# Performance work log

Measured on AMD Instinct MI355X. Metric: run time of the kernel, lower is better.

Reference implementation:

```python
import jax, jax.numpy as jnp
import numpy as np

B, S, D, H = 4, 2048, 1024, 16
HD = D // H  # head_dim = 64


def setup_inputs() -> dict:
    key = jax.random.key(0)
    ks = jax.random.split(key, 10)
    sc = 0.02
    return {
        "data": jax.random.normal(ks[0], (B, S, D), jnp.float32),
        "context": jax.random.normal(ks[1], (B, S, D), jnp.float32),
        "Wq": jax.random.normal(ks[2], (D, D), jnp.float32) * sc,
        "bq": jnp.zeros((D,), jnp.float32),
        "Wk": jax.random.normal(ks[3], (D, D), jnp.float32) * sc,
        "bk": jnp.zeros((D,), jnp.float32),
        "Wv": jax.random.normal(ks[4], (D, D), jnp.float32) * sc,
        "bv": jnp.zeros((D,), jnp.float32),
        "Wo": jax.random.normal(ks[5], (D, D), jnp.float32) * sc,
        "bo": jnp.zeros((D,), jnp.float32),
    }


def reference(data, context, Wq, bq, Wk, bk, Wv, bv, Wo, bo):
    # Q/K/V projections (nn.Linear: x @ W^T + b; here weights stored as [in, out])
    Q = data @ Wq + bq            # [B,S,D]
    K = context @ Wk + bk
    V = context @ Wv + bv
    # split heads -> [B,H,S,HD]
    Q = Q.reshape(B, S, H, HD).transpose(0, 2, 1, 3)
    K = K.reshape(B, S, H, HD).transpose(0, 2, 1, 3)
    V = V.reshape(B, S, H, HD).transpose(0, 2, 1, 3)
    scale = jnp.sqrt(jnp.asarray(HD, Q.dtype))
    Z = jnp.einsum("bhqd,bhkd->bhqk", Q, K) / scale   # [B,H,S,S]
    # causal mask: row >= col allowed
    row = jnp.arange(S)[:, None]
    col = jnp.arange(S)[None, :]
    Z = jnp.where(row >= col, Z, jnp.asarray(-jnp.inf, Z.dtype))
    Z = jax.nn.softmax(Z, axis=-1)
    out = jnp.einsum("bhqk,bhkd->bhqd", Z, V)         # [B,H,S,HD]
    out = out.transpose(0, 2, 1, 3).reshape(B, S, D)
    return out @ Wo + bo
```

## Files before the change

### kernel.cpp

```cpp
#include <hip/hip_runtime.h>
#include <hip/hip_bf16.h>

#define B_ 4
#define S_ 2048
#define D_ 1024
#define H_ 16
#define HD_ 64
#define M_ (B_*S_)
#define NTOK (M_*D_)

typedef __bf16 bf16;
typedef __bf16 bf16v4 __attribute__((ext_vector_type(4)));
typedef __bf16 bf16v8 __attribute__((ext_vector_type(8)));
typedef float f32x4 __attribute__((ext_vector_type(4)));
typedef float f32x16 __attribute__((ext_vector_type(16)));

#define GLDS(gp, lp) __builtin_amdgcn_global_load_lds( \
    (const __attribute__((address_space(1))) void*)(gp), \
    (__attribute__((address_space(3))) void*)(lp), 16, 0, 0)

__global__ void prep_kernel(const float* __restrict__ data, const float* __restrict__ ctx,
                            bf16* __restrict__ dataB, bf16* __restrict__ ctxB,
                            const float* __restrict__ W0, const float* __restrict__ W1,
                            const float* __restrict__ W2, const float* __restrict__ W3,
                            bf16* __restrict__ T0, bf16* __restrict__ T1,
                            bf16* __restrict__ T2, bf16* __restrict__ T3,
                            float s0) {
    int bid = blockIdx.x;
    if (bid < 8192) {
        int i = (bid * 256 + (int)threadIdx.x) * 8;
        const float* src; bf16* dst;
        if (i < NTOK) { src = data + i; dst = dataB + i; }
        else          { src = ctx + (i - NTOK); dst = ctxB + (i - NTOK); }
        const float4* p = reinterpret_cast<const float4*>(src);
        float4 x = p[0], y = p[1];
        bf16v8 o;
        o[0] = (bf16)x.x; o[1] = (bf16)x.y; o[2] = (bf16)x.z; o[3] = (bf16)x.w;
        o[4] = (bf16)y.x; o[5] = (bf16)y.y; o[6] = (bf16)y.z; o[7] = (bf16)y.w;
        *reinterpret_cast<bf16v8*>(dst) = o;
    } else {
        __shared__ float tile[32][33];
        int local = bid - 8192;
        int which = local >> 10;
        int rem = local & 1023;
        const float* W = which == 0 ? W0 : which == 1 ? W1 : which == 2 ? W2 : W3;
        bf16* Wt       = which == 0 ? T0 : which == 1 ? T1 : which == 2 ? T2 : T3;
        float scale    = which == 0 ? s0 : 1.f;
        int nb = (rem & 31) * 32, kb = (rem >> 5) * 32;
        int t = threadIdx.x;
        int c = t & 31, r0 = t >> 5;
        for (int i = 0; i < 4; ++i) {
            int r = r0 + i * 8;
            tile[r][c] = W[(size_t)(kb + r) * D_ + nb + c];
        }
        __syncthreads();
        for (int i = 0; i < 4; ++i) {
            int r = r0 + i * 8;
            Wt[(size_t)(nb + r) * D_ + kb + c] = (bf16)(tile[c][r] * scale);
        }
    }
}

__global__ __launch_bounds__(256) void gemm_qkvo_kernel(
        const bf16* __restrict__ dataB, const bf16* __restrict__ ctxB, const bf16* __restrict__ Ob,
        const bf16* __restrict__ WqT, const bf16* __restrict__ WkT,
        const bf16* __restrict__ WvT, const bf16* __restrict__ WoT,
        const float* __restrict__ bq, const float* __restrict__ bk,
        const float* __restrict__ bv, const float* __restrict__ bo,
        bf16* __restrict__ Qb, bf16* __restrict__ Kb, bf16* __restrict__ Vt,
        float* __restrict__ outp, float qscale, int zofs) {
    __shared__ bf16 Asm[128 * 64];
    __shared__ bf16 Bsm[128 * 64];
    int z = blockIdx.z + zofs;
    const bf16* A; const bf16* Bt; const float* bias; float bscale = 1.f;
    if (z == 0)      { A = dataB; Bt = WqT; bias = bq; bscale = qscale; }
    else if (z == 1) { A = ctxB;  Bt = WkT; bias = bk; }
    else if (z == 2) { A = ctxB;  Bt = WvT; bias = bv; }
    else             { A = Ob;    Bt = WoT; bias = bo; }

    int mb = blockIdx.x * 128, nb = blockIdx.y * 128;
    int t = threadIdx.x, l = t & 63, w = t >> 6;
    int wr = w >> 1, wc = w & 1;
    int lg = l >> 4, lr = l & 15;
    f32x4 acc[4][4] = {};
    int srow = t >> 3;
    int schk = t & 7;
    for (int k0 = 0; k0 < D_; k0 += 64) {
        __syncthreads();
        #pragma unroll
        for (int p = 0; p < 4; ++p) {
            int row = p * 32 + srow;
            int ca = schk ^ (row & 7);
            GLDS(&A[(size_t)(mb + row) * D_ + k0 + ca * 8], &Asm[(size_t)(p * 256 + t) * 8]);
            GLDS(&Bt[(size_t)(nb + row) * D_ + k0 + ca * 8], &Bsm[(size_t)(p * 256 + t) * 8]);
        }
        __syncthreads();
        #pragma unroll
        for (int kk = 0; kk < 2; ++kk) {
            bf16v8 af[4], bfv[4];
            #pragma unroll
            for (int i = 0; i < 4; ++i) {
                int ra = wr * 64 + i * 16 + lr;
                af[i]  = *(const bf16v8*)&Asm[ra * 64 + (((kk * 4 + lg) ^ (ra & 7)) * 8)];
                int rb = wc * 64 + i * 16 + lr;
                bfv[i] = *(const bf16v8*)&Bsm[rb * 64 + (((kk * 4 + lg) ^ (rb & 7)) * 8)];
            }
            #pragma unroll
            for (int i = 0; i < 4; ++i)
                #pragma unroll
                for (int j = 0; j < 4; ++j)
                    acc[i][j] = __builtin_amdgcn_mfma_f32_16x16x32_bf16(af[i], bfv[j], acc[i][j], 0, 0, 0);
        }
    }
    #pragma unroll
    for (int i = 0; i < 4; ++i)
        #pragma unroll
        for (int j = 0; j < 4; ++j) {
            int col = nb + wc * 64 + j * 16 + lr;
            float bvv = bias[col] * bscale;
            int row0 = mb + wr * 64 + i * 16 + lg * 4;
            if (z == 2) {
                int b = row0 >> 11, s = row0 & 2047;
                int bh = b * 16 + (col >> 6), hd = col & 63;
                bf16v4 ov;
                #pragma unroll
                for (int r = 0; r < 4; ++r) ov[r] = (bf16)(acc[i][j][r] + bvv);
                *(bf16v4*)&Vt[((size_t)bh * 64 + hd) * 2048 + s] = ov;
            } else if (z == 3) {
                #pragma unroll
                for (int r = 0; r < 4; ++r)
                    outp[(size_t)(row0 + r) * D_ + col] = acc[i][j][r] + bvv;
            } else {
                bf16* dst = (z == 0) ? Qb : Kb;
                #pragma unroll
                for (int r = 0; r < 4; ++r)
                    dst[(size_t)(row0 + r) * D_ + col] = (bf16)(acc[i][j][r] + bvv);
            }
        }
}

__global__ __launch_bounds__(256, 2) void attn_kernel(const bf16* __restrict__ Q,
                                                      const bf16* __restrict__ Kb,
                                                      const bf16* __restrict__ Vt,
                                                      bf16* __restrict__ O) {
    __shared__ bf16 Ksm[2][64 * 64];
    __shared__ bf16 Vsm[2][64 * 64];

    int id = (int)blockIdx.x;
    int bh = id & 63;
    int qi = (S_ / 128 - 1) - (id >> 6);
    int qb = qi * 128;
    int b = bh >> 4, h = bh & 15;
    int t = threadIdx.x, w = t >> 6, l = t & 63;
    int ln = l & 31, hi = l >> 5;
    int qwave = qb + w * 32;
    int q = qwave + ln;

    const bf16* kbase = Kb + (size_t)(b * S_) * D_ + h * HD_;
    const bf16* vbase = Vt + (size_t)bh * HD_ * S_;
    const bf16* qptr  = Q + (size_t)(b * S_ + q) * D_ + h * HD_;

    bf16v8 qf[4];
    #pragma unroll
    for (int c = 0; c < 4; ++c)
        qf[c] = *(const bf16v8*)(qptr + c * 16 + hi * 8);

    bf16v8 ones;
    #pragma unroll
    for (int e = 0; e < 8; ++e) ones[e] = (bf16)1.0f;

    f32x16 o0 = {}, o1 = {};
    f32x16 ls = {};

    int srow = t >> 3, schk = t & 7;
    int nT = 2 * qi + 2;

    auto stage = [&](int kv0, int bufsel) {
        #pragma unroll
        for (int p = 0; p < 2; ++p) {
            int row = p * 32 + srow;
            int cs = schk ^ (row & 7);
            GLDS(kbase + (size_t)(kv0 + row) * D_ + cs * 8, &Ksm[bufsel][p * 2048 + t * 8]);
            GLDS(vbase + (size_t)row * S_ + kv0 + cs * 8,   &Vsm[bufsel][p * 2048 + t * 8]);
        }
    };

    stage(0, 0);
    for (int tt = 0; tt < nT; ++tt) {
        int cur = tt & 1;
        int kv0 = tt * 64;
        __syncthreads();
        if (tt + 1 < nT) stage(kv0 + 64, cur ^ 1);
        if (kv0 > qwave + 31) continue;

        f32x16 st0 = {}, st1 = {};
        __builtin_amdgcn_s_setprio(1);
        #pragma unroll
        for (int c = 0; c < 4; ++c) {
            int r0 = ln;
            bf16v8 kf0 = *(const bf16v8*)&Ksm[cur][r0 * 64 + (((2 * c + hi) ^ (r0 & 7)) * 8)];
            st0 = __builtin_amdgcn_mfma_f32_32x32x16_bf16(kf0, qf[c], st0, 0, 0, 0);
            int r1 = 32 + ln;
            bf16v8 kf1 = *(const bf16v8*)&Ksm[cur][r1 * 64 + (((2 * c + hi) ^ (r1 & 7)) * 8)];
            st1 = __builtin_amdgcn_mfma_f32_32x32x16_bf16(kf1, qf[c], st1, 0, 0, 0);
        }
        __builtin_amdgcn_s_setprio(0);

        if (kv0 + 63 > qwave) {
            #pragma unroll
            for (int rg = 0; rg < 16; ++rg) {
                int kvo = (rg & 3) + 8 * (rg >> 2) + 4 * hi;
                if (kv0 + kvo > q)      st0[rg] = -__builtin_inff();
                if (kv0 + 32 + kvo > q) st1[rg] = -__builtin_inff();
            }
        }

        #pragma unroll
        for (int i = 0; i < 16; ++i) {
            st0[i] = __builtin_exp2f(st0[i]);
            st1[i] = __builtin_exp2f(st1[i]);
        }

        uint32_t x0[4][2], x1[4][2];
        #pragma unroll
        for (int j = 0; j < 4; ++j) {
            asm("v_cvt_pk_bf16_f32 %0, %1, %2" : "=v"(x0[j][0]) : "v"(st0[4*j+0]), "v"(st0[4*j+1]));
            asm("v_cvt_pk_bf16_f32 %0, %1, %2" : "=v"(x0[j][1]) : "v"(st0[4*j+2]), "v"(st0[4*j+3]));
            asm("v_cvt_pk_bf16_f32 %0, %1, %2" : "=v"(x1[j][0]) : "v"(st1[4*j+0]), "v"(st1[4*j+1]));
            asm("v_cvt_pk_bf16_f32 %0, %1, %2" : "=v"(x1[j][1]) : "v"(st1[4*j+2]), "v"(st1[4*j+3]));
        }
        union PB { uint32_t u[4]; bf16v8 v; };
        PB pb[4];
        #pragma unroll
        for (int c = 0; c < 4; ++c) {
            uint32_t (*xs)[2] = (c >> 1) ? x1 : x0;
            int cp = c & 1;
            #pragma unroll
            for (int d = 0; d < 2; ++d) {
                uint32_t own_lo = xs[2 * cp][d];
                uint32_t own_hi = xs[2 * cp + 1][d];
                uint32_t par_lo = __shfl_xor(own_lo, 32, 64);
                uint32_t par_hi = __shfl_xor(own_hi, 32, 64);
                pb[c].u[d]     = hi ? par_hi : own_lo;
                pb[c].u[2 + d] = hi ? own_hi : par_lo;
            }
        }

        __builtin_amdgcn_s_setprio(1);
        #pragma unroll
        for (int c = 0; c < 4; ++c) {
            int r0 = ln;
            bf16v8 va0 = *(const bf16v8*)&Vsm[cur][r0 * 64 + (((2 * c + hi) ^ (r0 & 7)) * 8)];
            o0 = __builtin_amdgcn_mfma_f32_32x32x16_bf16(va0, pb[c].v, o0, 0, 0, 0);
            int r1 = 32 + ln;
            bf16v8 va1 = *(const bf16v8*)&Vsm[cur][r1 * 64 + (((2 * c + hi) ^ (r1 & 7)) * 8)];
            o1 = __builtin_amdgcn_mfma_f32_32x32x16_bf16(va1, pb[c].v, o1, 0, 0, 0);
            ls = __builtin_amdgcn_mfma_f32_32x32x16_bf16(ones, pb[c].v, ls, 0, 0, 0);
        }
        __builtin_amdgcn_s_setprio(0);
    }

    float li = 1.f / ls[0];
    bf16* obase = O + (size_t)(b * S_ + q) * D_ + h * HD_;
    #pragma unroll
    for (int j = 0; j < 4; ++j) {
        bf16v4 ov;
        #pragma unroll
        for (int r = 0; r < 4; ++r) ov[r] = (bf16)(o0[4 * j + r] * li);
        *(bf16v4*)(obase + 8 * j + 4 * hi) = ov;
    }
    #pragma unroll
    for (int j = 0; j < 4; ++j) {
        bf16v4 ov;
        #pragma unroll
        for (int r = 0; r < 4; ++r) ov[r] = (bf16)(o1[4 * j + r] * li);
        *(bf16v4*)(obase + 32 + 8 * j + 4 * hi) = ov;
    }
}

extern "C" void kernel_launch(void* const* d_in, const int* in_sizes, int n_in,
                              void* d_out, int out_size, void* d_ws, size_t ws_size,
                              hipStream_t stream) {
    const float* data    = (const float*)d_in[0];
    const float* context = (const float*)d_in[1];
    const float* Wq = (const float*)d_in[2];
    const float* bq = (const float*)d_in[3];
    const float* Wk = (const float*)d_in[4];
    const float* bk = (const float*)d_in[5];
    const float* Wv = (const float*)d_in[6];
    const float* bv = (const float*)d_in[7];
    const float* Wo = (const float*)d_in[8];
    const float* bo = (const float*)d_in[9];
    float* out = (float*)d_out;

    char* ws = (char*)d_ws;
    size_t off = 0;
    auto alloc = [&](size_t bytes) { void* p = ws + off; off += (bytes + 255) & ~255ull; return p; };
    bf16* dataB = (bf16*)alloc((size_t)M_ * D_ * 2);
    bf16* ctxB  = (bf16*)alloc((size_t)M_ * D_ * 2);
    bf16* WqT   = (bf16*)alloc((size_t)D_ * D_ * 2);
    bf16* WkT   = (bf16*)alloc((size_t)D_ * D_ * 2);
    bf16* WvT   = (bf16*)alloc((size_t)D_ * D_ * 2);
    bf16* WoT   = (bf16*)alloc((size_t)D_ * D_ * 2);
    bf16* Qb    = (bf16*)alloc((size_t)M_ * D_ * 2);
    bf16* Kb    = (bf16*)alloc((size_t)M_ * D_ * 2);
    bf16* Vt    = (bf16*)alloc((size_t)M_ * D_ * 2);
    bf16* Ob    = ctxB;

    const float qscale = 0.125f * 1.44269504088896340736f;

    prep_kernel<<<12288, 256, 0, stream>>>(data, context, dataB, ctxB,
                                           Wq, Wk, Wv, Wo, WqT, WkT, WvT, WoT, qscale);

    gemm_qkvo_kernel<<<dim3(M_ / 128, D_ / 128, 3), 256, 0, stream>>>(
        dataB, ctxB, Ob, WqT, WkT, WvT, WoT, bq, bk, bv, bo, Qb, Kb, Vt, out, qscale, 0);

    attn_kernel<<<dim3(S_ / 128 * B_ * H_), 256, 0, stream>>>(Qb, Kb, Vt, Ob);

    gemm_qkvo_kernel<<<dim3(M_ / 128, D_ / 128, 1), 256, 0, stream>>>(
        dataB, ctxB, Ob, WqT, WkT, WvT, WoT, bq, bk, bv, bo, Qb, Kb, Vt, out, qscale, 3);
}
```

Measured before the change: 175.2 us.

## Add 256x256 double-buffered pipelined QKV GEMM with 8 waves

Replaces the QKV projection GEMM with a new kernel using 256x256 tiles, 512 threads and a double-buffered LDS pipeline. Async global-to-LDS loads are interleaved with MFMA phases, with explicit vmcnt waits, barriers and raised scheduling priority around the MFMA blocks. The intent is to hide memory latency and raise arithmetic intensity per block. The output projection moves to its own simpler kernel. The larger tiles use 128 KB of LDS per block and shrink the grid, which risks lower occupancy and tail imbalance, and the hand-written waitcnt counts must match the issued loads exactly.

Measured after the change: 186.0 us. +6.1%, slower.

```diff
diff --git a/kernel.cpp b/kernel.cpp
--- a/kernel.cpp
+++ b/kernel.cpp
@@ -61,23 +61,144 @@
     }
 }
 
-__global__ __launch_bounds__(256) void gemm_qkvo_kernel(
-        const bf16* __restrict__ dataB, const bf16* __restrict__ ctxB, const bf16* __restrict__ Ob,
-        const bf16* __restrict__ WqT, const bf16* __restrict__ WkT,
-        const bf16* __restrict__ WvT, const bf16* __restrict__ WoT,
-        const float* __restrict__ bq, const float* __restrict__ bk,
-        const float* __restrict__ bv, const float* __restrict__ bo,
-        bf16* __restrict__ Qb, bf16* __restrict__ Kb, bf16* __restrict__ Vt,
-        float* __restrict__ outp, float qscale, int zofs) {
+__global__ __launch_bounds__(512, 2) void gemm_qkv8_kernel(
+        const bf16* __restrict__ dataB, const bf16* __restrict__ ctxB,
+        const bf16* __restrict__ WqT, const bf16* __restrict__ WkT, const bf16* __restrict__ WvT,
+        const float* __restrict__ bq, const float* __restrict__ bk, const float* __restrict__ bv,
+        bf16* __restrict__ Qb, bf16* __restrict__ Kb, bf16* __restrict__ Vt, float qscale) {
+    __shared__ bf16 Asm[2][256 * 64];
+    __shared__ bf16 Bsm[2][256 * 64];
+    int z = blockIdx.z;
+    const bf16* A  = (z == 0) ? dataB : ctxB;
+    const bf16* Bt = (z == 0) ? WqT : (z == 1) ? WkT : WvT;
+    const float* bias = (z == 0) ? bq : (z == 1) ? bk : bv;
+    float bscale = (z == 0) ? qscale : 1.f;
+
+    int mb = blockIdx.x * 256, nb = blockIdx.y * 256;
+    int t = threadIdx.x, l = t & 63, w = t >> 6;
+    int wr = w >> 2, wc = w & 3;
+    int lg = l >> 4, lr = l & 15;
+    int srow = t >> 3, schk = t & 7;
+
+    f32x4 acc[2][2][4][2] = {};
+
+    auto stageA = [&](int tile, int g) {
+        int buf = tile & 1;
+        #pragma unroll
+        for (int p64 = 0; p64 < 2; ++p64) {
+            int row = p64 * 128 + g * 64 + srow;
+            int cs = schk ^ (row & 7);
+            GLDS(A + (size_t)(mb + row) * D_ + tile * 64 + cs * 8,
+                 &Asm[buf][row * 64 + schk * 8]);
+        }
+    };
+    auto stageB = [&](int tile, int g) {
+        int buf = tile & 1;
+        #pragma unroll
+        for (int p64 = 0; p64 < 2; ++p64) {
+            int v = p64 * 64 + srow;
+            int row = (v >> 5) * 64 + g * 32 + (v & 31);
+            int cs = schk ^ (row & 7);
+            GLDS(Bt + (size_t)(nb + row) * D_ + tile * 64 + cs * 8,
+                 &Bsm[buf][row * 64 + schk * 8]);
+        }
+    };
+
+    stageA(0, 0); stageB(0, 0); stageA(0, 1); stageB(0, 1); stageA(1, 0); stageB(1, 0);
+    asm volatile("s_waitcnt vmcnt(8)" ::: "memory");
+    __builtin_amdgcn_s_barrier();
+
+    for (int it = 0; it < 8; ++it) {
+        int b1 = 2 * it + 1, a2 = 2 * it + 2, b2 = 2 * it + 3;
+        #pragma unroll
+        for (int p = 0; p < 8; ++p) {
+            const int tsel = p >> 2;
+            const int qa = (p >> 1) & 1, qb = p & 1;
+
+            bf16v8 af[4][2], bfv[2][2];
+            #pragma unroll
+            for (int i4 = 0; i4 < 4; ++i4) {
+                int ra = wr * 128 + qa * 64 + i4 * 16 + lr;
+                #pragma unroll
+                for (int kk = 0; kk < 2; ++kk)
+                    af[i4][kk] = *(const bf16v8*)&Asm[tsel][ra * 64 + (((kk * 4 + lg) ^ (ra & 7)) * 8)];
+            }
+            #pragma unroll
+            for (int j2 = 0; j2 < 2; ++j2) {
+                int rb = wc * 64 + qb * 32 + j2 * 16 + lr;
+                #pragma unroll
+                for (int kk = 0; kk < 2; ++kk)
+                    bfv[j2][kk] = *(const bf16v8*)&Bsm[tsel][rb * 64 + (((kk * 4 + lg) ^ (rb & 7)) * 8)];
+            }
+
+            if (p == 0)      stageA(b1, 1);
+            else if (p == 1) stageB(b1, 1);
+            else if (p == 2) { if (a2 < 16) stageA(a2, 0); }
+            else if (p == 3) { if (a2 < 16) stageB(a2, 0); }
+            else if (p == 4) { if (a2 < 16) stageA(a2, 1); }
+            else if (p == 5) { if (a2 < 16) stageB(a2, 1); }
+            else if (p == 6) { if (b2 < 16) stageA(b2, 0); }
+            else             { if (b2 < 16) stageB(b2, 0); }
+
+            if (p == 0) asm volatile("s_waitcnt vmcnt(6)" ::: "memory");
+            if (p == 3) {
+                if (it == 7) asm volatile("s_waitcnt vmcnt(0)" ::: "memory");
+                else         asm volatile("s_waitcnt vmcnt(8)" ::: "memory");
+            }
+            if (p == 4 && it < 7) asm volatile("s_waitcnt vmcnt(6)" ::: "memory");
+            if (p == 7 && it < 7) asm volatile("s_waitcnt vmcnt(8)" ::: "memory");
+
+            __builtin_amdgcn_s_barrier();
+            asm volatile("s_waitcnt lgkmcnt(0)" ::: "memory");
+            __builtin_amdgcn_sched_barrier(0);
+            __builtin_amdgcn_s_setprio(1);
+            #pragma unroll
+            for (int kk = 0; kk < 2; ++kk)
+                #pragma unroll
+                for (int i4 = 0; i4 < 4; ++i4)
+                    #pragma unroll
+                    for (int j2 = 0; j2 < 2; ++j2)
+                        acc[qa][qb][i4][j2] = __builtin_amdgcn_mfma_f32_16x16x32_bf16(
+                            af[i4][kk], bfv[j2][kk], acc[qa][qb][i4][j2], 0, 0, 0);
+            __builtin_amdgcn_s_setprio(0);
+            __builtin_amdgcn_s_barrier();
+        }
+    }
+
+    #pragma unroll
+    for (int qa = 0; qa < 2; ++qa)
+        #pragma unroll
+        for (int qb = 0; qb < 2; ++qb)
+            #pragma unroll
+            for (int i4 = 0; i4 < 4; ++i4)
+                #pragma unroll
+                for (int j2 = 0; j2 < 2; ++j2) {
+                    int col = nb + wc * 64 + qb * 32 + j2 * 16 + lr;
+                    float bvv = bias[col] * bscale;
+                    int row0 = mb + wr * 128 + qa * 64 + i4 * 16 + lg * 4;
+                    f32x4 a = acc[qa][qb][i4][j2];
+                    if (z == 2) {
+                        int bb = row0 >> 11, s = row0 & 2047;
+                        int bh = bb * 16 + (col >> 6), hd = col & 63;
+                        bf16v4 ov;
+                        #pragma unroll
+                        for (int r = 0; r < 4; ++r) ov[r] = (bf16)(a[r] + bvv);
+                        *(bf16v4*)&Vt[((size_t)bh * 64 + hd) * 2048 + s] = ov;
+                    } else {
+                        bf16* dst = (z == 0) ? Qb : Kb;
+                        #pragma unroll
+                        for (int r = 0; r < 4; ++r)
+                            dst[(size_t)(row0 + r) * D_ + col] = (bf16)(a[r] + bvv);
+                    }
+                }
+}
+
+__global__ __launch_bounds__(256) void gemm_o_kernel(const bf16* __restrict__ Ob,
+                                                     const bf16* __restrict__ WoT,
+                                                     const float* __restrict__ bo,
+                                                     float* __restrict__ outp) {
     __shared__ bf16 Asm[128 * 64];
     __shared__ bf16 Bsm[128 * 64];
-    int z = blockIdx.z + zofs;
-    const bf16* A; const bf16* Bt; const float* bias; float bscale = 1.f;
-    if (z == 0)      { A = dataB; Bt = WqT; bias = bq; bscale = qscale; }
-    else if (z == 1) { A = ctxB;  Bt = WkT; bias = bk; }
-    else if (z == 2) { A = ctxB;  Bt = WvT; bias = bv; }
-    else             { A = Ob;    Bt = WoT; bias = bo; }
-
     int mb = blockIdx.x * 128, nb = blockIdx.y * 128;
     int t = threadIdx.x, l = t & 63, w = t >> 6;
     int wr = w >> 1, wc = w & 1;
@@ -91,8 +212,8 @@
         for (int p = 0; p < 4; ++p) {
             int row = p * 32 + srow;
             int ca = schk ^ (row & 7);
-            GLDS(&A[(size_t)(mb + row) * D_ + k0 + ca * 8], &Asm[(size_t)(p * 256 + t) * 8]);
-            GLDS(&Bt[(size_t)(nb + row) * D_ + k0 + ca * 8], &Bsm[(size_t)(p * 256 + t) * 8]);
+            GLDS(&Ob[(size_t)(mb + row) * D_ + k0 + ca * 8], &Asm[(size_t)(p * 256 + t) * 8]);
+            GLDS(&WoT[(size_t)(nb + row) * D_ + k0 + ca * 8], &Bsm[(size_t)(p * 256 + t) * 8]);
         }
         __syncthreads();
         #pragma unroll
@@ -117,25 +238,11 @@
         #pragma unroll
         for (int j = 0; j < 4; ++j) {
             int col = nb + wc * 64 + j * 16 + lr;
-            float bvv = bias[col] * bscale;
+            float bvv = bo[col];
             int row0 = mb + wr * 64 + i * 16 + lg * 4;
-            if (z == 2) {
-                int b = row0 >> 11, s = row0 & 2047;
-                int bh = b * 16 + (col >> 6), hd = col & 63;
-                bf16v4 ov;
-                #pragma unroll
-                for (int r = 0; r < 4; ++r) ov[r] = (bf16)(acc[i][j][r] + bvv);
-                *(bf16v4*)&Vt[((size_t)bh * 64 + hd) * 2048 + s] = ov;
-            } else if (z == 3) {
-                #pragma unroll
-                for (int r = 0; r < 4; ++r)
-                    outp[(size_t)(row0 + r) * D_ + col] = acc[i][j][r] + bvv;
-            } else {
-                bf16* dst = (z == 0) ? Qb : Kb;
-                #pragma unroll
-                for (int r = 0; r < 4; ++r)
-                    dst[(size_t)(row0 + r) * D_ + col] = (bf16)(acc[i][j][r] + bvv);
-            }
+            #pragma unroll
+            for (int r = 0; r < 4; ++r)
+                outp[(size_t)(row0 + r) * D_ + col] = acc[i][j][r] + bvv;
         }
 }
 
@@ -312,11 +419,10 @@
     prep_kernel<<<12288, 256, 0, stream>>>(data, context, dataB, ctxB,
                                            Wq, Wk, Wv, Wo, WqT, WkT, WvT, WoT, qscale);
 
-    gemm_qkvo_kernel<<<dim3(M_ / 128, D_ / 128, 3), 256, 0, stream>>>(
-        dataB, ctxB, Ob, WqT, WkT, WvT, WoT, bq, bk, bv, bo, Qb, Kb, Vt, out, qscale, 0);
+    gemm_qkv8_kernel<<<dim3(M_ / 256, D_ / 256, 3), 512, 0, stream>>>(
+        dataB, ctxB, WqT, WkT, WvT, bq, bk, bv, Qb, Kb, Vt, qscale);
 
     attn_kernel<<<dim3(S_ / 128 * B_ * H_), 256, 0, stream>>>(Qb, Kb, Vt, Ob);
 
-    gemm_qkvo_kernel<<<dim3(M_ / 128, D_ / 128, 1), 256, 0, stream>>>(
-        dataB, ctxB, Ob, WqT, WkT, WvT, WoT, bq, bk, bv, bo, Qb, Kb, Vt, out, qscale, 3);
+    gemm_o_kernel<<<dim3(M_ / 128, D_ / 128), 256, 0, stream>>>(Ob, WoT, bo, out);
 }
```

## Double query rows per wave in attention to reuse K/V fragments

Applied to the files above, without the earlier changes.

Each attention workgroup now covers 256 query rows instead of 128, and each wave handles two 32-row query sub-tiles that share every K and V fragment read from LDS. The aim is to halve the LDS reads and global K/V staging per query and to give the MFMA units more independent work to interleave. Block ordering is changed to a zigzag over the 8 query blocks. In exchange the grid shrinks to 512 workgroups, register pressure roughly doubles for accumulators (risking spills or lower occupancy under launch_bounds(256,2)), and causal imbalance per block grows.

Result: slower. 195.7 us (+11.7%).

```diff
diff --git a/kernel.cpp b/kernel.cpp
--- a/kernel.cpp
+++ b/kernel.cpp
@@ -148,32 +148,36 @@
 
     int id = (int)blockIdx.x;
     int bh = id & 63;
-    int qi = (S_ / 128 - 1) - (id >> 6);
-    int qb = qi * 128;
+    int g = id >> 6;
+    int qi = (g < 4) ? (7 - g) : (g - 4);
+    int qb = qi * 256;
     int b = bh >> 4, h = bh & 15;
     int t = threadIdx.x, w = t >> 6, l = t & 63;
     int ln = l & 31, hi = l >> 5;
-    int qwave = qb + w * 32;
-    int q = qwave + ln;
+    int qwave = qb + w * 64;
+    int qA = qwave + ln, qB = qwave + 32 + ln;
 
     const bf16* kbase = Kb + (size_t)(b * S_) * D_ + h * HD_;
     const bf16* vbase = Vt + (size_t)bh * HD_ * S_;
-    const bf16* qptr  = Q + (size_t)(b * S_ + q) * D_ + h * HD_;
-
-    bf16v8 qf[4];
+    const bf16* qptrA = Q + (size_t)(b * S_ + qA) * D_ + h * HD_;
+    const bf16* qptrB = Q + (size_t)(b * S_ + qB) * D_ + h * HD_;
+
+    bf16v8 qfA[4], qfB[4];
     #pragma unroll
-    for (int c = 0; c < 4; ++c)
-        qf[c] = *(const bf16v8*)(qptr + c * 16 + hi * 8);
+    for (int c = 0; c < 4; ++c) {
+        qfA[c] = *(const bf16v8*)(qptrA + c * 16 + hi * 8);
+        qfB[c] = *(const bf16v8*)(qptrB + c * 16 + hi * 8);
+    }
 
     bf16v8 ones;
     #pragma unroll
     for (int e = 0; e < 8; ++e) ones[e] = (bf16)1.0f;
 
-    f32x16 o0 = {}, o1 = {};
-    f32x16 ls = {};
+    f32x16 oA0 = {}, oA1 = {}, oB0 = {}, oB1 = {};
+    f32x16 lsA = {}, lsB = {};
 
     int srow = t >> 3, schk = t & 7;
-    int nT = 2 * qi + 2;
+    int nT = 4 * qi + 4;
 
     auto stage = [&](int kv0, int bufsel) {
         #pragma unroll
@@ -191,18 +195,20 @@
         int kv0 = tt * 64;
         __syncthreads();
         if (tt + 1 < nT) stage(kv0 + 64, cur ^ 1);
-        if (kv0 > qwave + 31) continue;
-
-        f32x16 st0 = {}, st1 = {};
+        if (kv0 > qwave + 63) continue;
+
+        f32x16 sA0 = {}, sA1 = {}, sB0 = {}, sB1 = {};
         __builtin_amdgcn_s_setprio(1);
         #pragma unroll
         for (int c = 0; c < 4; ++c) {
             int r0 = ln;
             bf16v8 kf0 = *(const bf16v8*)&Ksm[cur][r0 * 64 + (((2 * c + hi) ^ (r0 & 7)) * 8)];
-            st0 = __builtin_amdgcn_mfma_f32_32x32x16_bf16(kf0, qf[c], st0, 0, 0, 0);
+            sA0 = __builtin_amdgcn_mfma_f32_32x32x16_bf16(kf0, qfA[c], sA0, 0, 0, 0);
+            sB0 = __builtin_amdgcn_mfma_f32_32x32x16_bf16(kf0, qfB[c], sB0, 0, 0, 0);
             int r1 = 32 + ln;
             bf16v8 kf1 = *(const bf16v8*)&Ksm[cur][r1 * 64 + (((2 * c + hi) ^ (r1 & 7)) * 8)];
-            st1 = __builtin_amdgcn_mfma_f32_32x32x16_bf16(kf1, qf[c], st1, 0, 0, 0);
+            sA1 = __builtin_amdgcn_mfma_f32_32x32x16_bf16(kf1, qfA[c], sA1, 0, 0, 0);
+            sB1 = __builtin_amdgcn_mfma_f32_32x32x16_bf16(kf1, qfB[c], sB1, 0, 0, 0);
         }
         __builtin_amdgcn_s_setprio(0);
 
@@ -210,39 +216,69 @@
             #pragma unroll
             for (int rg = 0; rg < 16; ++rg) {
                 int kvo = (rg & 3) + 8 * (rg >> 2) + 4 * hi;
-                if (kv0 + kvo > q)      st0[rg] = -__builtin_inff();
-                if (kv0 + 32 + kvo > q) st1[rg] = -__builtin_inff();
+                if (kv0 + kvo > qA)      sA0[rg] = -__builtin_inff();
+                if (kv0 + 32 + kvo > qA) sA1[rg] = -__builtin_inff();
+                if (kv0 + kvo > qB)      sB0[rg] = -__builtin_inff();
+                if (kv0 + 32 + kvo > qB) sB1[rg] = -__builtin_inff();
             }
         }
 
         #pragma unroll
         for (int i = 0; i < 16; ++i) {
-            st0[i] = __builtin_exp2f(st0[i]);
-            st1[i] = __builtin_exp2f(st1[i]);
-        }
-
-        uint32_t x0[4][2], x1[4][2];
-        #pragma unroll
-        for (int j = 0; j < 4; ++j) {
-            asm("v_cvt_pk_bf16_f32 %0, %1, %2" : "=v"(x0[j][0]) : "v"(st0[4*j+0]), "v"(st0[4*j+1]));
-            asm("v_cvt_pk_bf16_f32 %0, %1, %2" : "=v"(x0[j][1]) : "v"(st0[4*j+2]), "v"(st0[4*j+3]));
-            asm("v_cvt_pk_bf16_f32 %0, %1, %2" : "=v"(x1[j][0]) : "v"(st1[4*j+0]), "v"(st1[4*j+1]));
-            asm("v_cvt_pk_bf16_f32 %0, %1, %2" : "=v"(x1[j][1]) : "v"(st1[4*j+2]), "v"(st1[4*j+3]));
-        }
+            sA0[i] = __builtin_exp2f(sA0[i]);
+            sA1[i] = __builtin_exp2f(sA1[i]);
+            sB0[i] = __builtin_exp2f(sB0[i]);
+            sB1[i] = __builtin_exp2f(sB1[i]);
+        }
+
         union PB { uint32_t u[4]; bf16v8 v; };
-        PB pb[4];
-        #pragma unroll
-        for (int c = 0; c < 4; ++c) {
-            uint32_t (*xs)[2] = (c >> 1) ? x1 : x0;
-            int cp = c & 1;
-            #pragma unroll
-            for (int d = 0; d < 2; ++d) {
-                uint32_t own_lo = xs[2 * cp][d];
-                uint32_t own_hi = xs[2 * cp + 1][d];
-                uint32_t par_lo = __shfl_xor(own_lo, 32, 64);
-                uint32_t par_hi = __shfl_xor(own_hi, 32, 64);
-                pb[c].u[d]     = hi ? par_hi : own_lo;
-                pb[c].u[2 + d] = hi ? own_hi : par_lo;
+        PB pbA[4], pbB[4];
+        {
+            uint32_t x0[4][2], x1[4][2];
+            #pragma unroll
+            for (int j = 0; j < 4; ++j) {
+                asm("v_cvt_pk_bf16_f32 %0, %1, %2" : "=v"(x0[j][0]) : "v"(sA0[4*j+0]), "v"(sA0[4*j+1]));
+                asm("v_cvt_pk_bf16_f32 %0, %1, %2" : "=v"(x0[j][1]) : "v"(sA0[4*j+2]), "v"(sA0[4*j+3]));
+                asm("v_cvt_pk_bf16_f32 %0, %1, %2" : "=v"(x1[j][0]) : "v"(sA1[4*j+0]), "v"(sA1[4*j+1]));
+                asm("v_cvt_pk_bf16_f32 %0, %1, %2" : "=v"(x1[j][1]) : "v"(sA1[4*j+2]), "v"(sA1[4*j+3]));
+            }
+            #pragma unroll
+            for (int c = 0; c < 4; ++c) {
+                uint32_t (*xs)[2] = (c >> 1) ? x1 : x0;
+                int cp = c & 1;
+                #pragma unroll
+                for (int d = 0; d < 2; ++d) {
+                    uint32_t own_lo = xs[2 * cp][d];
+                    uint32_t own_hi = xs[2 * cp + 1][d];
+                    uint32_t par_lo = __shfl_xor(own_lo, 32, 64);
+                    uint32_t par_hi = __shfl_xor(own_hi, 32, 64);
+                    pbA[c].u[d]     = hi ? par_hi : own_lo;
+                    pbA[c].u[2 + d] = hi ? own_hi : par_lo;
+                }
+            }
+        }
+        {
+            uint32_t x0[4][2], x1[4][2];
+            #pragma unroll
+            for (int j = 0; j < 4; ++j) {
+                asm("v_cvt_pk_bf16_f32 %0, %1, %2" : "=v"(x0[j][0]) : "v"(sB0[4*j+0]), "v"(sB0[4*j+1]));
+                asm("v_cvt_pk_bf16_f32 %0, %1, %2" : "=v"(x0[j][1]) : "v"(sB0[4*j+2]), "v"(sB0[4*j+3]));
+                asm("v_cvt_pk_bf16_f32 %0, %1, %2" : "=v"(x1[j][0]) : "v"(sB1[4*j+0]), "v"(sB1[4*j+1]));
+                asm("v_cvt_pk_bf16_f32 %0, %1, %2" : "=v"(x1[j][1]) : "v"(sB1[4*j+2]), "v"(sB1[4*j+3]));
+            }
+            #pragma unroll
+            for (int c = 0; c < 4; ++c) {
+                uint32_t (*xs)[2] = (c >> 1) ? x1 : x0;
+                int cp = c & 1;
+                #pragma unroll
+                for (int d = 0; d < 2; ++d) {
+                    uint32_t own_lo = xs[2 * cp][d];
+                    uint32_t own_hi = xs[2 * cp + 1][d];
+                    uint32_t par_lo = __shfl_xor(own_lo, 32, 64);
+                    uint32_t par_hi = __shfl_xor(own_hi, 32, 64);
+                    pbB[c].u[d]     = hi ? par_hi : own_lo;
+                    pbB[c].u[2 + d] = hi ? own_hi : par_lo;
+                }
             }
         }
 
@@ -251,30 +287,53 @@
         for (int c = 0; c < 4; ++c) {
             int r0 = ln;
             bf16v8 va0 = *(const bf16v8*)&Vsm[cur][r0 * 64 + (((2 * c + hi) ^ (r0 & 7)) * 8)];
-            o0 = __builtin_amdgcn_mfma_f32_32x32x16_bf16(va0, pb[c].v, o0, 0, 0, 0);
+            oA0 = __builtin_amdgcn_mfma_f32_32x32x16_bf16(va0, pbA[c].v, oA0, 0, 0, 0);
+            oB0 = __builtin_amdgcn_mfma_f32_32x32x16_bf16(va0, pbB[c].v, oB0, 0, 0, 0);
             int r1 = 32 + ln;
             bf16v8 va1 = *(const bf16v8*)&Vsm[cur][r1 * 64 + (((2 * c + hi) ^ (r1 & 7)) * 8)];
-            o1 = __builtin_amdgcn_mfma_f32_32x32x16_bf16(va1, pb[c].v, o1, 0, 0, 0);
-            ls = __builtin_amdgcn_mfma_f32_32x32x16_bf16(ones, pb[c].v, ls, 0, 0, 0);
+            oA1 = __builtin_amdgcn_mfma_f32_32x32x16_bf16(va1, pbA[c].v, oA1, 0, 0, 0);
+            oB1 = __builtin_amdgcn_mfma_f32_32x32x16_bf16(va1, pbB[c].v, oB1, 0, 0, 0);
+            lsA = __builtin_amdgcn_mfma_f32_32x32x16_bf16(ones, pbA[c].v, lsA, 0, 0, 0);
+            lsB = __builtin_amdgcn_mfma_f32_32x32x16_bf16(ones, pbB[c].v, lsB, 0, 0, 0);
         }
         __builtin_amdgcn_s_setprio(0);
     }
 
-    float li = 1.f / ls[0];
-    bf16* obase = O + (size_t)(b * S_ + q) * D_ + h * HD_;
-    #pragma unroll
-    for (int j = 0; j < 4; ++j) {
-        bf16v4 ov;
-        #pragma unroll
-        for (int r = 0; r < 4; ++r) ov[r] = (bf16)(o0[4 * j + r] * li);
-        *(bf16v4*)(obase + 8 * j + 4 * hi) = ov;
-    }
-    #pragma unroll
-    for (int j = 0; j < 4; ++j) {
-        bf16v4 ov;
-        #pragma unroll
-        for (int r = 0; r < 4; ++r) ov[r] = (bf16)(o1[4 * j + r] * li);
-        *(bf16v4*)(obase + 32 + 8 * j + 4 * hi) = ov;
+    {
+        float li = 1.f / lsA[0];
+        bf16* obase = O + (size_t)(b * S_ + qA) * D_ + h * HD_;
+        #pragma unroll
+        for (int j = 0; j < 4; ++j) {
+            bf16v4 ov;
+            #pragma unroll
+            for (int r = 0; r < 4; ++r) ov[r] = (bf16)(oA0[4 * j + r] * li);
+            *(bf16v4*)(obase + 8 * j + 4 * hi) = ov;
+        }
+        #pragma unroll
+        for (int j = 0; j < 4; ++j) {
+            bf16v4 ov;
+            #pragma unroll
+            for (int r = 0; r < 4; ++r) ov[r] = (bf16)(oA1[4 * j + r] * li);
+            *(bf16v4*)(obase + 32 + 8 * j + 4 * hi) = ov;
+        }
+    }
+    {
+        float li = 1.f / lsB[0];
+        bf16* obase = O + (size_t)(b * S_ + qB) * D_ + h * HD_;
+        #pragma unroll
+        for (int j = 0; j < 4; ++j) {
+            bf16v4 ov;
+            #pragma unroll
+            for (int r = 0; r < 4; ++r) ov[r] = (bf16)(oB0[4 * j + r] * li);
+            *(bf16v4*)(obase + 8 * j + 4 * hi) = ov;
+        }
+        #pragma unroll
+        for (int j = 0; j < 4; ++j) {
+            bf16v4 ov;
+            #pragma unroll
+            for (int r = 0; r < 4; ++r) ov[r] = (bf16)(oB1[4 * j + r] * li);
+            *(bf16v4*)(obase + 32 + 8 * j + 4 * hi) = ov;
+        }
     }
 }
 
@@ -315,7 +374,7 @@
     gemm_qkvo_kernel<<<dim3(M_ / 128, D_ / 128, 3), 256, 0, stream>>>(
         dataB, ctxB, Ob, WqT, WkT, WvT, WoT, bq, bk, bv, bo, Qb, Kb, Vt, out, qscale, 0);
 
-    attn_kernel<<<dim3(S_ / 128 * B_ * H_), 256, 0, stream>>>(Qb, Kb, Vt, Ob);
+    attn_kernel<<<dim3(S_ / 256 * B_ * H_), 256, 0, stream>>>(Qb, Kb, Vt, Ob);
 
     gemm_qkvo_kernel<<<dim3(M_ / 128, D_ / 128, 1), 256, 0, stream>>>(
         dataB, ctxB, Ob, WqT, WkT, WvT, WoT, bq, bk, bv, bo, Qb, Kb, Vt, out, qscale, 3);
```
